# Kernel tuning notes

Measured on AMD Instinct MI355X. Metric: run time of the kernel, lower is better.

The kernel has to match this reference:

```python
import jax, jax.numpy as jnp
import numpy as np

B, H, N, D, M = 4, 16, 4096, 64, 256
EPS = 1e-6


def setup_inputs() -> dict:
    key = jax.random.key(0)
    kq, kk, kv, kp = jax.random.split(key, 4)
    q = jax.random.normal(kq, (B, H, N, D), dtype=jnp.float32)
    k = jax.random.normal(kk, (B, H, N, D), dtype=jnp.float32)
    v = jax.random.normal(kv, (B, H, N, D), dtype=jnp.float32)
    # Orthogonal gaussian random-feature matrix [M, D], built like the torch module
    rng = np.random.default_rng(0)
    blocks = []
    n_blocks = M // D
    for _ in range(n_blocks):
        g = rng.standard_normal((D, D))
        qmat, _ = np.linalg.qr(g)
        blocks.append(qmat.T)
    rem = M - n_blocks * D
    if rem > 0:
        g = rng.standard_normal((D, D))
        qmat, _ = np.linalg.qr(g)
        blocks.append(qmat.T[:rem])
    mat = np.concatenate(blocks, axis=0)
    mult = rng.standard_normal((M,))
    proj_mat = jnp.asarray((mult[:, None] * mat).astype(np.float32))
    return {"q": q, "k": k, "v": v, "proj_mat": proj_mat}


def _feature_map(x, proj_mat):
    # x: [b,h,n,d], proj_mat: [m,d] -> [b,h,n,m]; GELU kernel (erf-based, torch default)
    scores = jnp.einsum('bhnd,md->bhnm', x, proj_mat)
    return jax.nn.gelu(scores, approximate=False) + EPS


def reference(q, k, v, proj_mat):
    qp = _feature_map(q, proj_mat)          # [b,h,n,m]
    kp = _feature_map(k, proj_mat)          # [b,h,n,m]
    k_sum = kp.sum(axis=-2)                 # [b,h,m]
    d_inv = 1.0 / jnp.einsum('bhnm,bhm->bhn', qp, k_sum)   # [b,h,n]
    contexts = jnp.einsum('bhnm,bhne->bhme', kp, v)         # [b,h,m,e]
    out = jnp.einsum('bhme,bhnm,bhn->bhne', contexts, qp, d_inv)  # [b,h,n,e]
    return out
```

## Files before the change

### kernel.cpp

```cpp
#include <hip/hip_runtime.h>
#include <cstdint>

#define BH    64
#define NSEQ  4096
#define DH    64
#define MF    256
#define RT    128
#define EPS   1e-6f

typedef float f32;
typedef __attribute__((ext_vector_type(4))) float f32x4;

__device__ __forceinline__ float gelu_eps(float x) {
    return 0.5f * x * (1.0f + erff(x * 0.70710678118654752f)) + EPS;
}

#define CTX_FLOATS (BH * MF * 64)
#define WS_FLOATS  (CTX_FLOATS + BH * MF)

__global__ void zero_ws_kernel(f32x4* __restrict__ p) {
    int i = blockIdx.x * 256 + threadIdx.x;
    p[i] = (f32x4){0.f, 0.f, 0.f, 0.f};
}

__global__ __launch_bounds__(256) void kside_kernel(
    const f32* __restrict__ Kg_, const f32* __restrict__ Vg_,
    const f32* __restrict__ Pg_, f32* __restrict__ ctx_ws,
    f32* __restrict__ ksum_ws)
{
    __shared__ f32x4 sV4[RT * 16];
    __shared__ f32x4 kp4[RT * 16];
    __shared__ f32x4 sP4[64 * 16];

    const int tid = threadIdx.x;
    const int bh  = blockIdx.x >> 3;
    const int cg  = blockIdx.x & 7;
    const int rg  = tid >> 3, fg = tid & 7;
    const int fq  = tid & 15, eg = tid >> 4;
    const size_t bhbase = (size_t)bh * NSEQ;

    f32x4 ctxacc[4][4];
    f32x4 ksacc[4];
    #pragma unroll
    for (int f = 0; f < 4; ++f) {
        ksacc[f] = (f32x4){0.f, 0.f, 0.f, 0.f};
        #pragma unroll
        for (int fi = 0; fi < 4; ++fi) ctxacc[f][fi] = (f32x4){0.f, 0.f, 0.f, 0.f};
    }

    for (int c = 0; c < 4; ++c) {
        const int rowbase = cg * 512 + c * 128;
        __syncthreads();
        const f32x4* Vg = (const f32x4*)(Vg_ + (bhbase + rowbase) * DH);
        #pragma unroll
        for (int p = 0; p < 8; ++p) sV4[tid + p * 256] = Vg[tid + p * 256];

        const f32* Kg = Kg_ + (bhbase + rowbase) * DH;

        #pragma unroll
        for (int f = 0; f < 4; ++f) {
            {
                const f32x4* Pg = (const f32x4*)(Pg_ + (size_t)f * 64 * DH);
                f32* base = (f32*)sP4;
                #pragma unroll
                for (int p = 0; p < 4; ++p) {
                    int m2 = tid + p * 256;
                    int feat = m2 >> 4, dq = m2 & 15;
                    f32x4 val = Pg[m2];
                    #pragma unroll
                    for (int jj = 0; jj < 4; ++jj) {
                        int d = dq * 4 + jj;
                        base[d * 64 + (((feat >> 2) ^ (d & 15)) << 2) + (feat & 3)] = val[jj];
                    }
                }
            }
            __syncthreads();

            f32x4 s0[4], s1[4];
            #pragma unroll
            for (int r = 0; r < 4; ++r) {
                s0[r] = (f32x4){0.f, 0.f, 0.f, 0.f};
                s1[r] = (f32x4){0.f, 0.f, 0.f, 0.f};
            }
            #pragma unroll 4
            for (int kb = 0; kb < 16; ++kb) {
                f32x4 a[4];
                #pragma unroll
                for (int r = 0; r < 4; ++r)
                    a[r] = *(const f32x4*)(Kg + (size_t)(rg * 4 + r) * DH + kb * 4);
                #pragma unroll
                for (int kk = 0; kk < 4; ++kk) {
                    int d = kb * 4 + kk;
                    f32x4 b0 = sP4[d * 16 + ((fg * 2)     ^ (d & 15))];
                    f32x4 b1 = sP4[d * 16 + ((fg * 2 + 1) ^ (d & 15))];
                    #pragma unroll
                    for (int r = 0; r < 4; ++r) {
                        s0[r] += a[r][kk] * b0;
                        s1[r] += a[r][kk] * b1;
                    }
                }
            }
            #pragma unroll
            for (int r = 0; r < 4; ++r) {
                int row = rg * 4 + r;
                f32x4 g0, g1;
                #pragma unroll
                for (int i = 0; i < 4; ++i) { g0[i] = gelu_eps(s0[r][i]); g1[i] = gelu_eps(s1[r][i]); }
                kp4[row * 16 + ((fg * 2)     ^ (row & 15))] = g0;
                kp4[row * 16 + ((fg * 2 + 1) ^ (row & 15))] = g1;
            }
            __syncthreads();

            #pragma unroll 4
            for (int rb = 0; rb < 32; ++rb) {
                f32x4 a4[4], b4[4];
                #pragma unroll
                for (int rr = 0; rr < 4; ++rr) {
                    int row = rb * 4 + rr;
                    a4[rr] = kp4[row * 16 + (fq ^ (row & 15))];
                    b4[rr] = sV4[row * 16 + eg];
                }
                #pragma unroll
                for (int rr = 0; rr < 4; ++rr) {
                    #pragma unroll
                    for (int fi = 0; fi < 4; ++fi)
                        ctxacc[f][fi] += a4[rr][fi] * b4[rr];
                }
                if (eg == 0) {
                    #pragma unroll
                    for (int rr = 0; rr < 4; ++rr) ksacc[f] += a4[rr];
                }
            }
        }
    }

    #pragma unroll
    for (int f = 0; f < 4; ++f) {
        f32* cb = ctx_ws + ((size_t)bh * MF + f * 64 + fq * 4) * 64 + eg * 4;
        #pragma unroll
        for (int fi = 0; fi < 4; ++fi)
            #pragma unroll
            for (int ei = 0; ei < 4; ++ei)
                atomicAdd(cb + (size_t)fi * 64 + ei, ctxacc[f][fi][ei]);
        if (eg == 0) {
            f32* kb_ = ksum_ws + (size_t)bh * MF + f * 64 + fq * 4;
            #pragma unroll
            for (int fi = 0; fi < 4; ++fi) atomicAdd(kb_ + fi, ksacc[f][fi]);
        }
    }
}

__global__ __launch_bounds__(256) void qside_kernel(
    const f32* __restrict__ Qg_, const f32* __restrict__ Pg_,
    const f32* __restrict__ ctx_ws, const f32* __restrict__ ksum_ws,
    f32* __restrict__ out)
{
    __shared__ f32x4 qp4[RT * 16];
    __shared__ f32x4 sU4[64 * 16];
    __shared__ f32x4 sks4[64];

    const int tid   = threadIdx.x;
    const int bh    = blockIdx.x >> 5;
    const int chunk = blockIdx.x & 31;
    const int rg = tid >> 3, fg = tid & 7;
    const size_t bhbase  = (size_t)bh * NSEQ;
    const int    rowbase = chunk * 128;

    if (tid < 64) sks4[tid] = ((const f32x4*)(ksum_ws + (size_t)bh * MF))[tid];

    const f32* Qg = Qg_ + (bhbase + rowbase) * DH;

    f32x4 num[4][2];
    float den[4] = {0.f, 0.f, 0.f, 0.f};
    #pragma unroll
    for (int r = 0; r < 4; ++r) { num[r][0] = (f32x4){0.f,0.f,0.f,0.f}; num[r][1] = (f32x4){0.f,0.f,0.f,0.f}; }

    for (int f = 0; f < 4; ++f) {
        __syncthreads();
        {
            const f32x4* Pg = (const f32x4*)(Pg_ + (size_t)f * 64 * DH);
            f32* base = (f32*)sU4;
            #pragma unroll
            for (int p = 0; p < 4; ++p) {
                int m2 = tid + p * 256;
                int feat = m2 >> 4, dq = m2 & 15;
                f32x4 val = Pg[m2];
                #pragma unroll
                for (int jj = 0; jj < 4; ++jj) {
                    int d = dq * 4 + jj;
                    base[d * 64 + (((feat >> 2) ^ (d & 15)) << 2) + (feat & 3)] = val[jj];
                }
            }
        }
        __syncthreads();

        f32x4 s0[4], s1[4];
        #pragma unroll
        for (int r = 0; r < 4; ++r) {
            s0[r] = (f32x4){0.f, 0.f, 0.f, 0.f};
            s1[r] = (f32x4){0.f, 0.f, 0.f, 0.f};
        }
        #pragma unroll 4
        for (int kb = 0; kb < 16; ++kb) {
            f32x4 a[4];
            #pragma unroll
            for (int r = 0; r < 4; ++r)
                a[r] = *(const f32x4*)(Qg + (size_t)(rg * 4 + r) * DH + kb * 4);
            #pragma unroll
            for (int kk = 0; kk < 4; ++kk) {
                int d = kb * 4 + kk;
                f32x4 b0 = sU4[d * 16 + ((fg * 2)     ^ (d & 15))];
                f32x4 b1 = sU4[d * 16 + ((fg * 2 + 1) ^ (d & 15))];
                #pragma unroll
                for (int r = 0; r < 4; ++r) {
                    s0[r] += a[r][kk] * b0;
                    s1[r] += a[r][kk] * b1;
                }
            }
        }
        #pragma unroll
        for (int r = 0; r < 4; ++r) {
            int row = rg * 4 + r;
            f32x4 g0, g1;
            #pragma unroll
            for (int i = 0; i < 4; ++i) { g0[i] = gelu_eps(s0[r][i]); g1[i] = gelu_eps(s1[r][i]); }
            qp4[row * 16 + ((fg * 2)     ^ (row & 15))] = g0;
            qp4[row * 16 + ((fg * 2 + 1) ^ (row & 15))] = g1;
        }
        __syncthreads();

        {
            const f32x4* Cg = (const f32x4*)(ctx_ws + ((size_t)bh * MF + f * 64) * 64);
            #pragma unroll
            for (int p = 0; p < 4; ++p) {
                int m2 = tid + p * 256;
                int feat = m2 >> 4, eq = m2 & 15;
                sU4[feat * 16 + (eq ^ (feat & 15))] = Cg[m2];
            }
        }
        __syncthreads();

        #pragma unroll 4
        for (int kb = 0; kb < 16; ++kb) {
            f32x4 a[4];
            #pragma unroll
            for (int r = 0; r < 4; ++r) {
                int row = rg * 4 + r;
                a[r] = qp4[row * 16 + (kb ^ (row & 15))];
            }
            f32x4 kv = sks4[f * 16 + kb];
            #pragma unroll
            for (int kk = 0; kk < 4; ++kk) {
                int k = kb * 4 + kk;
                f32x4 b0 = sU4[k * 16 + ((fg * 2)     ^ (k & 15))];
                f32x4 b1 = sU4[k * 16 + ((fg * 2 + 1) ^ (k & 15))];
                #pragma unroll
                for (int r = 0; r < 4; ++r) {
                    num[r][0] += a[r][kk] * b0;
                    num[r][1] += a[r][kk] * b1;
                }
            }
            #pragma unroll
            for (int r = 0; r < 4; ++r)
                den[r] += a[r][0] * kv[0] + a[r][1] * kv[1] + a[r][2] * kv[2] + a[r][3] * kv[3];
        }
    }

    #pragma unroll
    for (int r = 0; r < 4; ++r) {
        int row = rg * 4 + r;
        float dinv = 1.0f / den[r];
        f32x4 o0 = num[r][0] * dinv;
        f32x4 o1 = num[r][1] * dinv;
        f32* ob = out + (size_t)(bhbase + rowbase + row) * DH + fg * 8;
        *(f32x4*)(ob)     = o0;
        *(f32x4*)(ob + 4) = o1;
    }
}

extern "C" void kernel_launch(void* const* d_in, const int* in_sizes, int n_in,
                              void* d_out, int out_size, void* d_ws, size_t ws_size,
                              hipStream_t stream) {
    const f32* q    = (const f32*)d_in[0];
    const f32* k    = (const f32*)d_in[1];
    const f32* v    = (const f32*)d_in[2];
    const f32* proj = (const f32*)d_in[3];
    f32* out     = (f32*)d_out;
    f32* ctx_ws  = (f32*)d_ws;
    f32* ksum_ws = ctx_ws + CTX_FLOATS;

    const int nzero = WS_FLOATS / 4;
    hipLaunchKernelGGL(zero_ws_kernel, dim3(nzero / 256), dim3(256), 0, stream,
                       (f32x4*)d_ws);
    hipLaunchKernelGGL(kside_kernel, dim3(BH * 8), dim3(256), 0, stream,
                       k, v, proj, ctx_ws, ksum_ws);
    hipLaunchKernelGGL(qside_kernel, dim3(BH * 32), dim3(256), 0, stream,
                       q, proj, ctx_ws, ksum_ws, out);
}
```

Measured before the change: 982.9 us.

## Restructure feature-map kernels to 512 threads with per-block feature slices and fast GELU

Replaces erff with an Abramowitz-Stegun polynomial approximation using a hardware reciprocal and fast exp. The K-side kernel now gives each block one 64-feature slice and a quarter of the sequence, so it no longer re-stages the projection per chunk, and it reads V straight from global instead of through shared memory. The Q-side kernel uses 512 threads with one f32x4 of output per thread and reads context straight from global instead of staging it in LDS. The GELU approximation adds error of roughly 1e-7, and the larger blocks change occupancy and register pressure.

```diff
diff --git a/kernel.cpp b/kernel.cpp
--- a/kernel.cpp
+++ b/kernel.cpp
@@ -5,276 +5,222 @@
 #define NSEQ  4096
 #define DH    64
 #define MF    256
-#define RT    128
 #define EPS   1e-6f
 
 typedef float f32;
 typedef __attribute__((ext_vector_type(4))) float f32x4;
 
-__device__ __forceinline__ float gelu_eps(float x) {
-    return 0.5f * x * (1.0f + erff(x * 0.70710678118654752f)) + EPS;
-}
-
 #define CTX_FLOATS (BH * MF * 64)
 #define WS_FLOATS  (CTX_FLOATS + BH * MF)
 
+__device__ __forceinline__ float gelu_eps(float s) {
+    float x  = s * 0.70710678118654752f;
+    float ax = fabsf(x);
+    float t  = __builtin_amdgcn_rcpf(fmaf(0.3275911f, ax, 1.0f));
+    float p  = t * fmaf(t, fmaf(t, fmaf(t, fmaf(t, 1.061405429f, -1.453152027f),
+                                        1.421413741f), -0.284496736f), 0.254829592f);
+    float e  = __expf(-(ax * ax));
+    float er = copysignf(fmaf(-p, e, 1.0f), x);
+    return fmaf(0.5f * s, er, fmaf(0.5f, s, EPS));
+}
+
 __global__ void zero_ws_kernel(f32x4* __restrict__ p) {
-    int i = blockIdx.x * 256 + threadIdx.x;
-    p[i] = (f32x4){0.f, 0.f, 0.f, 0.f};
-}
-
-__global__ __launch_bounds__(256) void kside_kernel(
+    p[blockIdx.x * 256 + threadIdx.x] = (f32x4){0.f, 0.f, 0.f, 0.f};
+}
+
+__device__ __forceinline__ void stage_P(const f32* __restrict__ Pg_, int f, f32x4* sP4) {
+    const f32x4* Pg = (const f32x4*)(Pg_ + (size_t)f * 64 * DH);
+    f32* base = (f32*)sP4;
+    #pragma unroll
+    for (int p = 0; p < 2; ++p) {
+        int m2 = threadIdx.x + p * 512;
+        int feat = m2 >> 4, dq = m2 & 15;
+        f32x4 val = Pg[m2];
+        #pragma unroll
+        for (int jj = 0; jj < 4; ++jj) {
+            int d = dq * 4 + jj;
+            base[d * 64 + (((feat >> 2) ^ (d & 15)) << 2) + (feat & 3)] = val[jj];
+        }
+    }
+}
+
+__global__ __launch_bounds__(512, 4) void kside_kernel(
     const f32* __restrict__ Kg_, const f32* __restrict__ Vg_,
     const f32* __restrict__ Pg_, f32* __restrict__ ctx_ws,
     f32* __restrict__ ksum_ws)
 {
-    __shared__ f32x4 sV4[RT * 16];
-    __shared__ f32x4 kp4[RT * 16];
     __shared__ f32x4 sP4[64 * 16];
+    __shared__ f32x4 kp4[128 * 16];
 
     const int tid = threadIdx.x;
-    const int bh  = blockIdx.x >> 3;
-    const int cg  = blockIdx.x & 7;
-    const int rg  = tid >> 3, fg = tid & 7;
-    const int fq  = tid & 15, eg = tid >> 4;
-    const size_t bhbase = (size_t)bh * NSEQ;
-
-    f32x4 ctxacc[4][4];
-    f32x4 ksacc[4];
-    #pragma unroll
-    for (int f = 0; f < 4; ++f) {
-        ksacc[f] = (f32x4){0.f, 0.f, 0.f, 0.f};
-        #pragma unroll
-        for (int fi = 0; fi < 4; ++fi) ctxacc[f][fi] = (f32x4){0.f, 0.f, 0.f, 0.f};
-    }
-
-    for (int c = 0; c < 4; ++c) {
-        const int rowbase = cg * 512 + c * 128;
-        __syncthreads();
-        const f32x4* Vg = (const f32x4*)(Vg_ + (bhbase + rowbase) * DH);
-        #pragma unroll
-        for (int p = 0; p < 8; ++p) sV4[tid + p * 256] = Vg[tid + p * 256];
-
-        const f32* Kg = Kg_ + (bhbase + rowbase) * DH;
-
-        #pragma unroll
-        for (int f = 0; f < 4; ++f) {
-            {
-                const f32x4* Pg = (const f32x4*)(Pg_ + (size_t)f * 64 * DH);
-                f32* base = (f32*)sP4;
-                #pragma unroll
-                for (int p = 0; p < 4; ++p) {
-                    int m2 = tid + p * 256;
-                    int feat = m2 >> 4, dq = m2 & 15;
-                    f32x4 val = Pg[m2];
-                    #pragma unroll
-                    for (int jj = 0; jj < 4; ++jj) {
-                        int d = dq * 4 + jj;
-                        base[d * 64 + (((feat >> 2) ^ (d & 15)) << 2) + (feat & 3)] = val[jj];
-                    }
-                }
-            }
-            __syncthreads();
-
-            f32x4 s0[4], s1[4];
-            #pragma unroll
-            for (int r = 0; r < 4; ++r) {
-                s0[r] = (f32x4){0.f, 0.f, 0.f, 0.f};
-                s1[r] = (f32x4){0.f, 0.f, 0.f, 0.f};
-            }
-            #pragma unroll 4
-            for (int kb = 0; kb < 16; ++kb) {
-                f32x4 a[4];
-                #pragma unroll
-                for (int r = 0; r < 4; ++r)
-                    a[r] = *(const f32x4*)(Kg + (size_t)(rg * 4 + r) * DH + kb * 4);
-                #pragma unroll
-                for (int kk = 0; kk < 4; ++kk) {
-                    int d = kb * 4 + kk;
-                    f32x4 b0 = sP4[d * 16 + ((fg * 2)     ^ (d & 15))];
-                    f32x4 b1 = sP4[d * 16 + ((fg * 2 + 1) ^ (d & 15))];
-                    #pragma unroll
-                    for (int r = 0; r < 4; ++r) {
-                        s0[r] += a[r][kk] * b0;
-                        s1[r] += a[r][kk] * b1;
-                    }
-                }
-            }
-            #pragma unroll
-            for (int r = 0; r < 4; ++r) {
-                int row = rg * 4 + r;
-                f32x4 g0, g1;
-                #pragma unroll
-                for (int i = 0; i < 4; ++i) { g0[i] = gelu_eps(s0[r][i]); g1[i] = gelu_eps(s1[r][i]); }
-                kp4[row * 16 + ((fg * 2)     ^ (row & 15))] = g0;
-                kp4[row * 16 + ((fg * 2 + 1) ^ (row & 15))] = g1;
-            }
-            __syncthreads();
-
-            #pragma unroll 4
-            for (int rb = 0; rb < 32; ++rb) {
-                f32x4 a4[4], b4[4];
-                #pragma unroll
-                for (int rr = 0; rr < 4; ++rr) {
-                    int row = rb * 4 + rr;
-                    a4[rr] = kp4[row * 16 + (fq ^ (row & 15))];
-                    b4[rr] = sV4[row * 16 + eg];
-                }
-                #pragma unroll
-                for (int rr = 0; rr < 4; ++rr) {
-                    #pragma unroll
-                    for (int fi = 0; fi < 4; ++fi)
-                        ctxacc[f][fi] += a4[rr][fi] * b4[rr];
-                }
-                if (eg == 0) {
-                    #pragma unroll
-                    for (int rr = 0; rr < 4; ++rr) ksacc[f] += a4[rr];
-                }
-            }
-        }
-    }
-
-    #pragma unroll
-    for (int f = 0; f < 4; ++f) {
-        f32* cb = ctx_ws + ((size_t)bh * MF + f * 64 + fq * 4) * 64 + eg * 4;
-        #pragma unroll
-        for (int fi = 0; fi < 4; ++fi)
-            #pragma unroll
-            for (int ei = 0; ei < 4; ++ei)
-                atomicAdd(cb + (size_t)fi * 64 + ei, ctxacc[f][fi][ei]);
-        if (eg == 0) {
-            f32* kb_ = ksum_ws + (size_t)bh * MF + f * 64 + fq * 4;
-            #pragma unroll
-            for (int fi = 0; fi < 4; ++fi) atomicAdd(kb_ + fi, ksacc[f][fi]);
-        }
-    }
-}
-
-__global__ __launch_bounds__(256) void qside_kernel(
+    const int bh  = blockIdx.x >> 4;
+    const int f   = (blockIdx.x >> 2) & 3;
+    const int rg  = blockIdx.x & 3;
+    const size_t rowbase0 = (size_t)bh * NSEQ + rg * 1024;
+
+    const int srg = tid >> 4, sfg = tid & 15;
+    const int h   = tid >> 8;
+    const int t8  = tid & 255;
+    const int cfq = t8 & 15, ceg = t8 >> 4;
+
+    stage_P(Pg_, f, sP4);
+    __syncthreads();
+
+    f32x4 ctxacc[4];
+    f32x4 ksacc = (f32x4){0.f, 0.f, 0.f, 0.f};
+    #pragma unroll
+    for (int fi = 0; fi < 4; ++fi) ctxacc[fi] = (f32x4){0.f, 0.f, 0.f, 0.f};
+
+    for (int t = 0; t < 8; ++t) {
+        const f32* Kg = Kg_ + (rowbase0 + t * 128) * DH;
+
+        f32x4 s[4];
+        #pragma unroll
+        for (int r = 0; r < 4; ++r) s[r] = (f32x4){0.f, 0.f, 0.f, 0.f};
+        #pragma unroll 4
+        for (int kb = 0; kb < 16; ++kb) {
+            f32x4 a[4];
+            #pragma unroll
+            for (int r = 0; r < 4; ++r)
+                a[r] = *(const f32x4*)(Kg + (size_t)(srg * 4 + r) * DH + kb * 4);
+            #pragma unroll
+            for (int kk = 0; kk < 4; ++kk) {
+                int d = kb * 4 + kk;
+                f32x4 b = sP4[d * 16 + (sfg ^ (d & 15))];
+                #pragma unroll
+                for (int r = 0; r < 4; ++r) s[r] += a[r][kk] * b;
+            }
+        }
+        #pragma unroll
+        for (int r = 0; r < 4; ++r) {
+            int row = srg * 4 + r;
+            f32x4 g;
+            #pragma unroll
+            for (int i = 0; i < 4; ++i) g[i] = gelu_eps(s[r][i]);
+            kp4[row * 16 + (sfg ^ (row & 15))] = g;
+        }
+        __syncthreads();
+
+        const f32* Vg = Vg_ + (rowbase0 + t * 128 + h * 64) * DH;
+        #pragma unroll 2
+        for (int rb = 0; rb < 16; ++rb) {
+            f32x4 a4[4], b4[4];
+            #pragma unroll
+            for (int rr = 0; rr < 4; ++rr) {
+                int row = h * 64 + rb * 4 + rr;
+                a4[rr] = kp4[row * 16 + (cfq ^ (row & 15))];
+                b4[rr] = *(const f32x4*)(Vg + (size_t)(rb * 4 + rr) * DH + ceg * 4);
+            }
+            #pragma unroll
+            for (int rr = 0; rr < 4; ++rr)
+                #pragma unroll
+                for (int fi = 0; fi < 4; ++fi)
+                    ctxacc[fi] += a4[rr][fi] * b4[rr];
+            if (ceg == 0) {
+                #pragma unroll
+                for (int rr = 0; rr < 4; ++rr) ksacc += a4[rr];
+            }
+        }
+        __syncthreads();
+    }
+
+    f32* cb = ctx_ws + ((size_t)bh * MF + f * 64 + cfq * 4) * 64 + ceg * 4;
+    #pragma unroll
+    for (int fi = 0; fi < 4; ++fi)
+        #pragma unroll
+        for (int ei = 0; ei < 4; ++ei)
+            atomicAdd(cb + (size_t)fi * 64 + ei, ctxacc[fi][ei]);
+    if (ceg == 0) {
+        f32* kb_ = ksum_ws + (size_t)bh * MF + f * 64 + cfq * 4;
+        #pragma unroll
+        for (int fi = 0; fi < 4; ++fi) atomicAdd(kb_ + fi, ksacc[fi]);
+    }
+}
+
+__global__ __launch_bounds__(512, 4) void qside_kernel(
     const f32* __restrict__ Qg_, const f32* __restrict__ Pg_,
     const f32* __restrict__ ctx_ws, const f32* __restrict__ ksum_ws,
     f32* __restrict__ out)
 {
-    __shared__ f32x4 qp4[RT * 16];
-    __shared__ f32x4 sU4[64 * 16];
-    __shared__ f32x4 sks4[64];
-
-    const int tid   = threadIdx.x;
-    const int bh    = blockIdx.x >> 5;
-    const int chunk = blockIdx.x & 31;
-    const int rg = tid >> 3, fg = tid & 7;
-    const size_t bhbase  = (size_t)bh * NSEQ;
-    const int    rowbase = chunk * 128;
-
-    if (tid < 64) sks4[tid] = ((const f32x4*)(ksum_ws + (size_t)bh * MF))[tid];
-
-    const f32* Qg = Qg_ + (bhbase + rowbase) * DH;
-
-    f32x4 num[4][2];
+    __shared__ f32x4 qp4[128 * 16];
+    __shared__ f32x4 sP4[64 * 16];
+    __shared__ f32x4 sks[64];
+
+    const int tid = threadIdx.x;
+    const int bh  = blockIdx.x >> 5;
+    const int ch  = blockIdx.x & 31;
+    const size_t rowbase = (size_t)bh * NSEQ + ch * 128;
+
+    const int srg = tid >> 4, sfg = tid & 15;
+    const int org = tid >> 4, oeg = tid & 15;
+
+    if (tid < 64) sks[tid] = ((const f32x4*)(ksum_ws + (size_t)bh * MF))[tid];
+
+    const f32* Qg = Qg_ + rowbase * DH;
+
+    f32x4 num[4];
     float den[4] = {0.f, 0.f, 0.f, 0.f};
     #pragma unroll
-    for (int r = 0; r < 4; ++r) { num[r][0] = (f32x4){0.f,0.f,0.f,0.f}; num[r][1] = (f32x4){0.f,0.f,0.f,0.f}; }
+    for (int r = 0; r < 4; ++r) num[r] = (f32x4){0.f, 0.f, 0.f, 0.f};
 
     for (int f = 0; f < 4; ++f) {
-        __syncthreads();
-        {
-            const f32x4* Pg = (const f32x4*)(Pg_ + (size_t)f * 64 * DH);
-            f32* base = (f32*)sU4;
-            #pragma unroll
-            for (int p = 0; p < 4; ++p) {
-                int m2 = tid + p * 256;
-                int feat = m2 >> 4, dq = m2 & 15;
-                f32x4 val = Pg[m2];
-                #pragma unroll
-                for (int jj = 0; jj < 4; ++jj) {
-                    int d = dq * 4 + jj;
-                    base[d * 64 + (((feat >> 2) ^ (d & 15)) << 2) + (feat & 3)] = val[jj];
-                }
-            }
-        }
-        __syncthreads();
-
-        f32x4 s0[4], s1[4];
-        #pragma unroll
-        for (int r = 0; r < 4; ++r) {
-            s0[r] = (f32x4){0.f, 0.f, 0.f, 0.f};
-            s1[r] = (f32x4){0.f, 0.f, 0.f, 0.f};
-        }
+        stage_P(Pg_, f, sP4);
+        __syncthreads();
+
+        f32x4 s[4];
+        #pragma unroll
+        for (int r = 0; r < 4; ++r) s[r] = (f32x4){0.f, 0.f, 0.f, 0.f};
         #pragma unroll 4
         for (int kb = 0; kb < 16; ++kb) {
             f32x4 a[4];
             #pragma unroll
             for (int r = 0; r < 4; ++r)
-                a[r] = *(const f32x4*)(Qg + (size_t)(rg * 4 + r) * DH + kb * 4);
+                a[r] = *(const f32x4*)(Qg + (size_t)(srg * 4 + r) * DH + kb * 4);
             #pragma unroll
             for (int kk = 0; kk < 4; ++kk) {
                 int d = kb * 4 + kk;
-                f32x4 b0 = sU4[d * 16 + ((fg * 2)     ^ (d & 15))];
-                f32x4 b1 = sU4[d * 16 + ((fg * 2 + 1) ^ (d & 15))];
-                #pragma unroll
-                for (int r = 0; r < 4; ++r) {
-                    s0[r] += a[r][kk] * b0;
-                    s1[r] += a[r][kk] * b1;
-                }
+                f32x4 b = sP4[d * 16 + (sfg ^ (d & 15))];
+                #pragma unroll
+                for (int r = 0; r < 4; ++r) s[r] += a[r][kk] * b;
             }
         }
         #pragma unroll
         for (int r = 0; r < 4; ++r) {
-            int row = rg * 4 + r;
-            f32x4 g0, g1;
-            #pragma unroll
-            for (int i = 0; i < 4; ++i) { g0[i] = gelu_eps(s0[r][i]); g1[i] = gelu_eps(s1[r][i]); }
-            qp4[row * 16 + ((fg * 2)     ^ (row & 15))] = g0;
-            qp4[row * 16 + ((fg * 2 + 1) ^ (row & 15))] = g1;
-        }
-        __syncthreads();
-
-        {
-            const f32x4* Cg = (const f32x4*)(ctx_ws + ((size_t)bh * MF + f * 64) * 64);
-            #pragma unroll
-            for (int p = 0; p < 4; ++p) {
-                int m2 = tid + p * 256;
-                int feat = m2 >> 4, eq = m2 & 15;
-                sU4[feat * 16 + (eq ^ (feat & 15))] = Cg[m2];
-            }
-        }
-        __syncthreads();
-
-        #pragma unroll 4
+            int row = srg * 4 + r;
+            f32x4 g;
+            #pragma unroll
+            for (int i = 0; i < 4; ++i) g[i] = gelu_eps(s[r][i]);
+            qp4[row * 16 + (sfg ^ (row & 15))] = g;
+        }
+        __syncthreads();
+
+        const f32* Cg = ctx_ws + ((size_t)bh * MF + f * 64) * 64;
+        #pragma unroll 2
         for (int kb = 0; kb < 16; ++kb) {
             f32x4 a[4];
             #pragma unroll
             for (int r = 0; r < 4; ++r) {
-                int row = rg * 4 + r;
+                int row = org * 4 + r;
                 a[r] = qp4[row * 16 + (kb ^ (row & 15))];
             }
-            f32x4 kv = sks4[f * 16 + kb];
+            f32x4 ks = sks[f * 16 + kb];
             #pragma unroll
             for (int kk = 0; kk < 4; ++kk) {
-                int k = kb * 4 + kk;
-                f32x4 b0 = sU4[k * 16 + ((fg * 2)     ^ (k & 15))];
-                f32x4 b1 = sU4[k * 16 + ((fg * 2 + 1) ^ (k & 15))];
-                #pragma unroll
-                for (int r = 0; r < 4; ++r) {
-                    num[r][0] += a[r][kk] * b0;
-                    num[r][1] += a[r][kk] * b1;
-                }
+                f32x4 b = *(const f32x4*)(Cg + (size_t)(kb * 4 + kk) * 64 + oeg * 4);
+                #pragma unroll
+                for (int r = 0; r < 4; ++r) num[r] += a[r][kk] * b;
             }
             #pragma unroll
             for (int r = 0; r < 4; ++r)
-                den[r] += a[r][0] * kv[0] + a[r][1] * kv[1] + a[r][2] * kv[2] + a[r][3] * kv[3];
+                den[r] += a[r][0] * ks[0] + a[r][1] * ks[1] + a[r][2] * ks[2] + a[r][3] * ks[3];
         }
     }
 
     #pragma unroll
     for (int r = 0; r < 4; ++r) {
-        int row = rg * 4 + r;
+        int row = org * 4 + r;
         float dinv = 1.0f / den[r];
-        f32x4 o0 = num[r][0] * dinv;
-        f32x4 o1 = num[r][1] * dinv;
-        f32* ob = out + (size_t)(bhbase + rowbase + row) * DH + fg * 8;
-        *(f32x4*)(ob)     = o0;
-        *(f32x4*)(ob + 4) = o1;
+        *(f32x4*)(out + (rowbase + row) * DH + oeg * 4) = num[r] * dinv;
     }
 }
 
@@ -292,8 +238,8 @@
     const int nzero = WS_FLOATS / 4;
     hipLaunchKernelGGL(zero_ws_kernel, dim3(nzero / 256), dim3(256), 0, stream,
                        (f32x4*)d_ws);
-    hipLaunchKernelGGL(kside_kernel, dim3(BH * 8), dim3(256), 0, stream,
+    hipLaunchKernelGGL(kside_kernel, dim3(BH * 16), dim3(512), 0, stream,
                        k, v, proj, ctx_ws, ksum_ws);
-    hipLaunchKernelGGL(qside_kernel, dim3(BH * 32), dim3(256), 0, stream,
+    hipLaunchKernelGGL(qside_kernel, dim3(BH * 32), dim3(512), 0, stream,
                        q, proj, ctx_ws, ksum_ws, out);
 }
```

After: 1.035 ms. +5.3%, slower.
